# Kernel tuning notes

Measured on AMD Instinct MI355X. Metric: run time of the kernel, lower is better.

## Reference

```python
import jax, jax.numpy as jnp
import numpy as np

N, E, H = 50000, 500000, 4
DIN, DH, DO, TD = 135, 128, 64, 9

def _ln(x, g, b):
    mu = jnp.mean(x, axis=-1, keepdims=True)
    v = jnp.var(x, axis=-1, keepdims=True)
    return (x - mu) / jnp.sqrt(v + 1e-5) * g + b

def _gat(x, src, dst, W, a_src, a_dst, b, n, heads, c):
    h = (x @ W).reshape(n, heads, c)                      # [N,H,C]
    es = jnp.sum(h * a_src, -1)                           # [N,H]
    ed = jnp.sum(h * a_dst, -1)
    e = jax.nn.leaky_relu(es[src] + ed[dst], 0.2)         # [E,H]
    m = jax.ops.segment_max(e, dst, num_segments=n)       # segment softmax over dst
    ex = jnp.exp(e - m[dst])
    den = jax.ops.segment_sum(ex, dst, num_segments=n)
    alpha = ex / (den[dst] + 1e-16)
    out = jax.ops.segment_sum(h[src] * alpha[..., None], dst, num_segments=n)
    return jnp.mean(out, axis=1) + b                      # concat=False -> head mean

def setup_inputs() -> dict:
    key = jax.random.key(0)
    ks = jax.random.split(key, 32)
    rn = lambda i, shape: jax.random.normal(ks[i], shape, jnp.float32) * 0.05
    inp = {}
    inp['x'] = jax.random.normal(ks[0], (N, DIN), jnp.float32)
    inp['edge_index'] = jax.random.randint(ks[1], (2, E), 0, N, jnp.int32)
    inp['edge_attr'] = jnp.ones((E, 1), jnp.float32)
    inp['W_in'] = rn(2, (DIN, DH)); inp['b_in'] = jnp.zeros((DH,), jnp.float32)
    inp['g1W'] = rn(3, (DH, H * DH)); inp['g1as'] = rn(4, (H, DH)); inp['g1ad'] = rn(5, (H, DH)); inp['g1b'] = jnp.zeros((DH,), jnp.float32)
    inp['g2W'] = rn(6, (DH, H * DH)); inp['g2as'] = rn(7, (H, DH)); inp['g2ad'] = rn(8, (H, DH)); inp['g2b'] = jnp.zeros((DH,), jnp.float32)
    inp['g3W'] = rn(9, (DH, H * DO)); inp['g3as'] = rn(10, (H, DO)); inp['g3ad'] = rn(11, (H, DO)); inp['g3b'] = jnp.zeros((DO,), jnp.float32)
    inp['r1W'] = rn(12, (DH, DH)); inp['r1b'] = jnp.zeros((DH,), jnp.float32)
    inp['r2W'] = rn(13, (DH, DH)); inp['r2b'] = jnp.zeros((DH,), jnp.float32)
    inp['r3W'] = rn(14, (DH, DO)); inp['r3b'] = jnp.zeros((DO,), jnp.float32)
    inp['n1g'] = jnp.ones((DH,), jnp.float32); inp['n1b'] = jnp.zeros((DH,), jnp.float32)
    inp['n2g'] = jnp.ones((DH,), jnp.float32); inp['n2b'] = jnp.zeros((DH,), jnp.float32)
    inp['n3g'] = jnp.ones((DO,), jnp.float32); inp['n3b'] = jnp.zeros((DO,), jnp.float32)
    inp['tw'] = jnp.float32(0.3)
    inp['c1W'] = rn(15, (DO, DO)); inp['c1b'] = jnp.zeros((DO,), jnp.float32)
    inp['clg'] = jnp.ones((DO,), jnp.float32); inp['clb'] = jnp.zeros((DO,), jnp.float32)
    inp['c2W'] = rn(16, (DO, 2)); inp['c2b'] = jnp.zeros((2,), jnp.float32)
    return inp

def reference(x, edge_index, edge_attr, W_in, b_in, g1W, g1as, g1ad, g1b,
              g2W, g2as, g2ad, g2b, g3W, g3as, g3ad, g3b,
              r1W, r1b, r2W, r2b, r3W, r3b,
              n1g, n1b, n2g, n2b, n3g, n3b, tw,
              c1W, c1b, clg, clb, c2W, c2b):
    n = x.shape[0]
    src0, dst0 = edge_index[0], edge_index[1]
    loop = jnp.arange(n, dtype=edge_index.dtype)          # GATConv add_self_loops=True
    src = jnp.concatenate([src0, loop])
    dst = jnp.concatenate([dst0, loop])
    # vectorized temporal cosine similarity over original edges
    t = x[:, -TD:]
    ti, tj = t[src0], t[dst0]
    nrm = jnp.maximum(jnp.linalg.norm(ti, axis=-1), 1e-8) * jnp.maximum(jnp.linalg.norm(tj, axis=-1), 1e-8)
    sim = jnp.sum(ti * tj, -1) / nrm
    scale = 1.0 + 0.1 * jnp.mean(1.0 + tw * sim)
    h = x @ W_in + b_in
    id1 = h
    h = _gat(h, src, dst, g1W, g1as, g1ad, g1b, n, H, DH) * scale
    h = _ln(jax.nn.relu(h) + id1 @ r1W + r1b, n1g, n1b)
    id2 = h
    h = _gat(h, src, dst, g2W, g2as, g2ad, g2b, n, H, DH) * scale
    h = _ln(jax.nn.relu(h) + id2 @ r2W + r2b, n2g, n2b)
    id3 = h
    h = _gat(h, src, dst, g3W, g3as, g3ad, g3b, n, H, DO)
    h = _ln(jax.nn.relu(h) + id3 @ r3W + r3b, n3g, n3b)
    ego = h[0:1]
    z = jax.nn.relu(ego @ c1W + c1b)
    z = _ln(z, clg, clb)
    return z @ c2W + c2b
```

## Files before the change

kernel.cpp:

```cpp
#include <hip/hip_runtime.h>

#define AGENT __HIP_MEMORY_SCOPE_AGENT

constexpr int TD = 9, DIN = 135;
constexpr int CAP3 = 256, CAP2 = 1024, CAP1 = 4096, BK = 128;
constexpr int NB = 512;
constexpr int LSTRIDE = 32;
constexpr int NGRP = 16, GSZ = 32;
constexpr int NSET = 8;
constexpr int NLINE = 64;

struct P {
  const float* x; const int* src; const int* dst; int N; int E;
  const float *W_in,*b_in,*g1W,*g1as,*g1ad,*g1b,*g2W,*g2as,*g2ad,*g2b,*g3W,*g3as,*g3ad,*g3b;
  const float *r1W,*r1b,*r2W,*r2b,*r3W,*r3b,*n1g,*n1b,*n2g,*n2b,*n3g,*n3b;
  const float *tw,*c1W,*c1b,*clg,*clb,*c2W,*c2b;
  float* tp;
  int *m3,*m2,*m1,*list3,*list2,*list1,*cnts;
  int *barc,*barr,*barg;
  int *bcnt1,*bcnt2,*bcnt3,*bk1,*bk2,*bk3;
  float *h0,*hh1,*es1,*ed1,*h1,*hh2,*es2,*ed2,*h2,*hh3,*es3,*ed3,*h3;
  float* dout;
};

__device__ __forceinline__ float lrelu(float v) { return v >= 0.f ? v : 0.2f * v; }

__device__ __forceinline__ void stg(float* pp, float v) { __hip_atomic_store(pp, v, __ATOMIC_RELAXED, AGENT); }
__device__ __forceinline__ void stg(int* pp, int v)   { __hip_atomic_store(pp, v, __ATOMIC_RELAXED, AGENT); }

__device__ __forceinline__ void claim_node(int v, int* __restrict__ m, int* __restrict__ list,
                                           int* __restrict__ cnt, int cap) {
  if (atomicCAS(&m[v], -1, -2) == -1) {
    int pos = atomicAdd(cnt, 1);
    if (pos < cap) { stg(&list[pos], v); stg(&m[v], pos); } else { stg(&m[v], -3); }
  }
}

__device__ __forceinline__ void grid_barrier(const P& p, int& lgen, int* amroot_s) {
  __syncthreads();
  int g = lgen + 1;
  if (threadIdx.x == 0) {
    *amroot_s = 0;
    int grp = blockIdx.x & (NGRP - 1);
    int* gc = &p.barc[(((g & (NSET - 1)) * NGRP) + grp) * LSTRIDE];
    if (__hip_atomic_fetch_add(gc, 1, __ATOMIC_RELAXED, AGENT) == GSZ - 1) {
      int* rc = &p.barr[(g & (NSET - 1)) * LSTRIDE];
      if (__hip_atomic_fetch_add(rc, 1, __ATOMIC_RELAXED, AGENT) == NGRP - 1) *amroot_s = 1;
    }
  }
  __syncthreads();
  if (*amroot_s) {
    if (threadIdx.x < NLINE)
      __hip_atomic_store(&p.barg[threadIdx.x * LSTRIDE], g, __ATOMIC_RELAXED, AGENT);
  } else if (threadIdx.x == 0) {
    int* line = &p.barg[(blockIdx.x & (NLINE - 1)) * LSTRIDE];
    while (__hip_atomic_load(line, __ATOMIC_RELAXED, AGENT) < g)
      __builtin_amdgcn_s_sleep(8);
  }
  __syncthreads();
  lgen = g;
}

__global__ void k_init(P p) {
  int gt = blockIdx.x * blockDim.x + threadIdx.x;
  int GT = gridDim.x * blockDim.x;
  int n3 = 3 * p.N;
  int4* mv = (int4*)p.m3;
  int4 neg = make_int4(-1, -1, -1, -1);
  int nv = n3 >> 2;
  for (int i = gt; i < nv; i += GT) mv[i] = neg;
  for (int i = (nv << 2) + gt; i < n3; i += GT) p.m3[i] = -1;
  if (gt < 64) p.cnts[gt] = 0;
  for (int i = gt; i < NSET * NGRP * LSTRIDE; i += GT) p.barc[i] = 0;
  for (int i = gt; i < NSET * LSTRIDE; i += GT) p.barr[i] = 0;
  for (int i = gt; i < NLINE * LSTRIDE; i += GT) p.barg[i] = 0;
  for (int i = gt; i < CAP2; i += GT) p.bcnt1[i] = 0;
  for (int i = gt; i < CAP3; i += GT) p.bcnt2[i] = 0;
  if (gt == 0) p.bcnt3[0] = 0;
  int total = p.N * TD;
  for (int i = gt; i < total; i += GT) {
    int v = i / TD, k = i - v * TD;
    p.tp[i] = p.x[(size_t)v * DIN + (DIN - TD) + k];
  }
}

template <int C, int ONEXT>
__device__ void gat_phase(int nq, const int* lst, const int* mPrev,
                          const int* bket, const int* bcnt,
                          const float* hh, const float* es, const float* ed, const float* hres,
                          const float* gb, const float* rW, const float* rb,
                          const float* ng, const float* nbv, float scale,
                          float* hout, const float* Wn, const float* avn, const float* bvn,
                          float* hhn, float* esn, float* edn,
                          float* elog, int* eposs, float* sh, float* hres_s, float* shln,
                          float* psn, float* pdn, float* sc2, float* ev_s) {
  const int T = 256, Wd = 4 * C, R = Wd / T;
  int tid = threadIdx.x;
  for (int q = blockIdx.x; q < nq; q += gridDim.x) {
    int v = lst[q];
    int sp = mPrev[v];
    int nb = min(bcnt[q], BK);
    for (int j = tid; j < nb; j += T) {
      int pu = mPrev[bket[(size_t)q * BK + j]];
      eposs[j] = pu;
      const float* ep = &es[(size_t)pu * 4];
      elog[0 * BK + j] = ep[0]; elog[1 * BK + j] = ep[1];
      elog[2 * BK + j] = ep[2]; elog[3 * BK + j] = ep[3];
    }
    if (tid < 4) { ev_s[tid] = es[(size_t)sp * 4 + tid]; ev_s[4 + tid] = ed[(size_t)sp * 4 + tid]; }
    for (int k = tid; k < 128; k += T) hres_s[k] = hres[(size_t)sp * 128 + k];
    __syncthreads();
#pragma unroll
    for (int r = 0; r < R; r++) {
      int w = r * T + tid, a = w / C;
      float edv = ev_s[4 + a];
      float eself = lrelu(ev_s[a] + edv);
      float mx = eself;
      for (int j = 0; j < nb; j++) mx = fmaxf(mx, lrelu(elog[a * BK + j] + edv));
      float den = __expf(eself - mx);
      for (int j = 0; j < nb; j++) den += __expf(lrelu(elog[a * BK + j] + edv) - mx);
      float rden = 1.f / (den + 1e-16f);
      float s = __expf(eself - mx) * rden * hh[(size_t)sp * Wd + w];
      for (int j = 0; j < nb; j++)
        s += __expf(lrelu(elog[a * BK + j] + edv) - mx) * rden * hh[(size_t)eposs[j] * Wd + w];
      sh[w] = s;
    }
    __syncthreads();
    float val = 0.f;
    if (tid < C) {
      float g = 0.25f * (sh[tid] + sh[C + tid] + sh[2 * C + tid] + sh[3 * C + tid]) + gb[tid];
      g *= scale;
      g = fmaxf(g, 0.f);
      float rr = rb[tid];
      for (int k = 0; k < 128; k++) rr += hres_s[k] * rW[(size_t)k * C + tid];
      val = g + rr;
      shln[tid] = val;
    }
    __syncthreads();
    if (tid == 0) {
      float s1 = 0.f, s2 = 0.f;
      for (int k = 0; k < C; k++) { float u = shln[k]; s1 += u; s2 += u * u; }
      float mu = s1 / (float)C;
      sc2[0] = mu;
      sc2[1] = rsqrtf(fmaxf(s2 / (float)C - mu * mu, 0.f) + 1e-5f);
    }
    __syncthreads();
    if (tid < C) {
      float o = (val - sc2[0]) * sc2[1] * ng[tid] + nbv[tid];
      stg(&hout[(size_t)q * C + tid], o);
      shln[tid] = o;
    }
    __syncthreads();
    if (ONEXT > 0) {
      for (int j = tid; j < ONEXT; j += T) {
        float a2 = 0.f;
        for (int k = 0; k < C; k++) a2 += shln[k] * Wn[(size_t)k * ONEXT + j];
        stg(&hhn[(size_t)q * ONEXT + j], a2);
        psn[j] = a2 * avn[j]; pdn[j] = a2 * bvn[j];
      }
      __syncthreads();
      if (tid < 8) {
        const int CN = ONEXT / 4; int a = tid & 3;
        const float* pr = (tid < 4) ? psn : pdn;
        float s = 0.f;
        for (int c = 0; c < CN; c++) s += pr[a * CN + c];
        stg(&(tid < 4 ? esn : edn)[(size_t)q * 4 + a], s);
      }
    }
    __syncthreads();
  }
}

__global__ __launch_bounds__(256, 2) void k_mega(P p) {
  __shared__ float elog[4 * BK];
  __shared__ int   eposs[BK];
  __shared__ float sh[512];
  __shared__ float hres_s[128];
  __shared__ float shln[128];
  __shared__ float psn[512], pdn[512];
  __shared__ float xs[DIN + 1];
  __shared__ float sc2[2];
  __shared__ float ev_s[8];
  __shared__ float wred[4];
  __shared__ float zcl[64];
  __shared__ int   amroot_s;

  int tid = threadIdx.x, bid = blockIdx.x;
  int gt = bid * 256 + tid, GT = gridDim.x * 256;
  int lgen = 0;
  float* simsum = (float*)&p.cnts[8];

  {
    if (gt == 0) claim_node(0, p.m3, p.list3, &p.cnts[0], CAP3);
    float local = 0.f;
    for (int e = gt; e < p.E; e += GT) {
      int s = p.src[e], d = p.dst[e];
      if (d == 0) claim_node(s, p.m3, p.list3, &p.cnts[0], CAP3);
      const float* ti = p.tp + (size_t)s * TD;
      const float* tj = p.tp + (size_t)d * TD;
      float dot = 0.f, na = 0.f, nb2 = 0.f;
#pragma unroll
      for (int k = 0; k < TD; k++) { float a = ti[k], b = tj[k]; dot += a * b; na += a * a; nb2 += b * b; }
      local += dot / (fmaxf(sqrtf(na), 1e-8f) * fmaxf(sqrtf(nb2), 1e-8f));
    }
    for (int off = 32; off > 0; off >>= 1) local += __shfl_down(local, off, 64);
    if ((tid & 63) == 0) wred[tid >> 6] = local;
    __syncthreads();
    if (tid == 0) atomicAdd(simsum, wred[0] + wred[1] + wred[2] + wred[3]);
  }
  grid_barrier(p, lgen, &amroot_s);

  {
    int c3 = min(__hip_atomic_load(&p.cnts[0], __ATOMIC_RELAXED, AGENT), CAP3);
    for (int i = gt; i < c3; i += GT) claim_node(p.list3[i], p.m2, p.list2, &p.cnts[1], CAP2);
    for (int e = gt; e < p.E; e += GT)
      if (p.m3[p.dst[e]] >= 0) claim_node(p.src[e], p.m2, p.list2, &p.cnts[1], CAP2);
  }
  grid_barrier(p, lgen, &amroot_s);

  {
    int c2 = min(__hip_atomic_load(&p.cnts[1], __ATOMIC_RELAXED, AGENT), CAP2);
    for (int i = gt; i < c2; i += GT) claim_node(p.list2[i], p.m1, p.list1, &p.cnts[2], CAP1);
    for (int e = gt; e < p.E; e += GT) {
      int s = p.src[e], d = p.dst[e];
      int p2 = p.m2[d];
      if (p2 >= 0) {
        claim_node(s, p.m1, p.list1, &p.cnts[2], CAP1);
        int sl = atomicAdd(&p.bcnt1[p2], 1); if (sl < BK) stg(&p.bk1[(size_t)p2 * BK + sl], s);
      }
      int p3 = p.m3[d];
      if (p3 >= 0) { int sl = atomicAdd(&p.bcnt2[p3], 1); if (sl < BK) stg(&p.bk2[(size_t)p3 * BK + sl], s); }
      if (d == 0)  { int sl = atomicAdd(&p.bcnt3[0], 1);  if (sl < BK) stg(&p.bk3[sl], s); }
    }
  }
  grid_barrier(p, lgen, &amroot_s);

  {
    int c1 = min(__hip_atomic_load(&p.cnts[2], __ATOMIC_RELAXED, AGENT), CAP1);
    for (int pp = bid; pp < c1; pp += gridDim.x) {
      int v = p.list1[pp];
      for (int k = tid; k < DIN; k += 256) xs[k] = p.x[(size_t)v * DIN + k];
      __syncthreads();
      if (tid < 128) {
        float acc = p.b_in[tid];
        for (int k = 0; k < DIN; k++) acc += xs[k] * p.W_in[(size_t)k * 128 + tid];
        stg(&p.h0[(size_t)pp * 128 + tid], acc);
        hres_s[tid] = acc;
      }
      __syncthreads();
#pragma unroll
      for (int jj = 0; jj < 2; jj++) {
        int j = jj * 256 + tid;
        float acc = 0.f;
        for (int k = 0; k < 128; k++) acc += hres_s[k] * p.g1W[(size_t)k * 512 + j];
        stg(&p.hh1[(size_t)pp * 512 + j], acc);
        psn[j] = acc * p.g1as[j]; pdn[j] = acc * p.g1ad[j];
      }
      __syncthreads();
      if (tid < 8) {
        int a = tid & 3;
        const float* pr = (tid < 4) ? psn : pdn;
        float s = 0.f;
        for (int c = 0; c < 128; c++) s += pr[a * 128 + c];
        stg(&(tid < 4 ? p.es1 : p.ed1)[(size_t)pp * 4 + a], s);
      }
      __syncthreads();
    }
  }
  grid_barrier(p, lgen, &amroot_s);

  int sbits = __hip_atomic_load(&p.cnts[8], __ATOMIC_RELAXED, AGENT);
  float scale = 1.1f + 0.1f * p.tw[0] * __int_as_float(sbits) / (float)p.E;

  {
    int c2 = min(__hip_atomic_load(&p.cnts[1], __ATOMIC_RELAXED, AGENT), CAP2);
    gat_phase<128, 512>(c2, p.list2, p.m1, p.bk1, p.bcnt1,
                        p.hh1, p.es1, p.ed1, p.h0,
                        p.g1b, p.r1W, p.r1b, p.n1g, p.n1b, scale,
                        p.h1, p.g2W, p.g2as, p.g2ad, p.hh2, p.es2, p.ed2,
                        elog, eposs, sh, hres_s, shln, psn, pdn, sc2, ev_s);
  }
  grid_barrier(p, lgen, &amroot_s);

  {
    int c3 = min(__hip_atomic_load(&p.cnts[0], __ATOMIC_RELAXED, AGENT), CAP3);
    gat_phase<128, 256>(c3, p.list3, p.m2, p.bk2, p.bcnt2,
                        p.hh2, p.es2, p.ed2, p.h1,
                        p.g2b, p.r2W, p.r2b, p.n2g, p.n2b, scale,
                        p.h2, p.g3W, p.g3as, p.g3ad, p.hh3, p.es3, p.ed3,
                        elog, eposs, sh, hres_s, shln, psn, pdn, sc2, ev_s);
  }
  grid_barrier(p, lgen, &amroot_s);

  {
    gat_phase<64, 0>(1, &p.cnts[56] , p.m3, p.bk3, p.bcnt3,
                     p.hh3, p.es3, p.ed3, p.h2,
                     p.g3b, p.r3W, p.r3b, p.n3g, p.n3b, 1.f,
                     p.h3, nullptr, nullptr, nullptr, nullptr, nullptr, nullptr,
                     elog, eposs, sh, hres_s, shln, psn, pdn, sc2, ev_s);
    if (bid == 0) {
      if (tid < 64) {
        float az = p.c1b[tid];
        for (int k = 0; k < 64; k++) az += shln[k] * p.c1W[k * 64 + tid];
        zcl[tid] = fmaxf(az, 0.f);
      }
      __syncthreads();
      if (tid == 0) {
        float s1 = 0.f, s2 = 0.f;
        for (int k = 0; k < 64; k++) { float u = zcl[k]; s1 += u; s2 += u * u; }
        float mu = s1 / 64.f;
        float rstd = rsqrtf(fmaxf(s2 / 64.f - mu * mu, 0.f) + 1e-5f);
        float o0 = p.c2b[0], o1 = p.c2b[1];
        for (int k = 0; k < 64; k++) {
          float zn = (zcl[k] - mu) * rstd * p.clg[k] + p.clb[k];
          o0 += zn * p.c2W[k * 2 + 0];
          o1 += zn * p.c2W[k * 2 + 1];
        }
        p.dout[0] = o0; p.dout[1] = o1;
      }
    }
  }
}

extern "C" void kernel_launch(void* const* d_in, const int* in_sizes, int n_in,
                              void* d_out, int out_size, void* d_ws, size_t ws_size,
                              hipStream_t stream) {
  P p;
  p.x = (const float*)d_in[0];
  const int* ei = (const int*)d_in[1];
  p.N = in_sizes[0] / DIN;
  p.E = in_sizes[1] / 2;
  p.src = ei; p.dst = ei + p.E;
  p.W_in = (const float*)d_in[3]; p.b_in = (const float*)d_in[4];
  p.g1W = (const float*)d_in[5]; p.g1as = (const float*)d_in[6]; p.g1ad = (const float*)d_in[7]; p.g1b = (const float*)d_in[8];
  p.g2W = (const float*)d_in[9]; p.g2as = (const float*)d_in[10]; p.g2ad = (const float*)d_in[11]; p.g2b = (const float*)d_in[12];
  p.g3W = (const float*)d_in[13]; p.g3as = (const float*)d_in[14]; p.g3ad = (const float*)d_in[15]; p.g3b = (const float*)d_in[16];
  p.r1W = (const float*)d_in[17]; p.r1b = (const float*)d_in[18];
  p.r2W = (const float*)d_in[19]; p.r2b = (const float*)d_in[20];
  p.r3W = (const float*)d_in[21]; p.r3b = (const float*)d_in[22];
  p.n1g = (const float*)d_in[23]; p.n1b = (const float*)d_in[24];
  p.n2g = (const float*)d_in[25]; p.n2b = (const float*)d_in[26];
  p.n3g = (const float*)d_in[27]; p.n3b = (const float*)d_in[28];
  p.tw  = (const float*)d_in[29];
  p.c1W = (const float*)d_in[30]; p.c1b = (const float*)d_in[31];
  p.clg = (const float*)d_in[32]; p.clb = (const float*)d_in[33];
  p.c2W = (const float*)d_in[34]; p.c2b = (const float*)d_in[35];
  p.dout = (float*)d_out;

  char* B = (char*)d_ws;
  size_t off = 0;
  auto take = [&](size_t nbytes) -> char* {
    char* r = B + off;
    off += (nbytes + 255) & ~(size_t)255;
    return r;
  };
  p.cnts  = (int*)take(256);
  p.barc  = (int*)take((size_t)NSET * NGRP * LSTRIDE * 4);
  p.barr  = (int*)take((size_t)NSET * LSTRIDE * 4);
  p.barg  = (int*)take((size_t)NLINE * LSTRIDE * 4);
  p.m3    = (int*)take((size_t)3 * p.N * 4);
  p.m2 = p.m3 + p.N; p.m1 = p.m2 + p.N;
  p.tp    = (float*)take((size_t)p.N * TD * 4);
  p.list3 = (int*)take(CAP3 * 4);
  p.list2 = (int*)take(CAP2 * 4);
  p.list1 = (int*)take(CAP1 * 4);
  p.bcnt1 = (int*)take(CAP2 * 4);
  p.bcnt2 = (int*)take(CAP3 * 4);
  p.bcnt3 = (int*)take(64);
  p.bk1   = (int*)take((size_t)CAP2 * BK * 4);
  p.bk2   = (int*)take((size_t)CAP3 * BK * 4);
  p.bk3   = (int*)take(BK * 4);
  p.h0    = (float*)take((size_t)CAP1 * 128 * 4);
  p.hh1   = (float*)take((size_t)CAP1 * 512 * 4);
  p.es1   = (float*)take((size_t)CAP1 * 16);
  p.ed1   = (float*)take((size_t)CAP1 * 16);
  p.h1    = (float*)take((size_t)CAP2 * 128 * 4);
  p.hh2   = (float*)take((size_t)CAP2 * 512 * 4);
  p.es2   = (float*)take((size_t)CAP2 * 16);
  p.ed2   = (float*)take((size_t)CAP2 * 16);
  p.h2    = (float*)take((size_t)CAP3 * 128 * 4);
  p.hh3   = (float*)take((size_t)CAP3 * 256 * 4);
  p.es3   = (float*)take((size_t)CAP3 * 16);
  p.ed3   = (float*)take((size_t)CAP3 * 16);
  p.h3    = (float*)take(64 * 4);

  k_init<<<1024, 256, 0, stream>>>(p);
  k_mega<<<NB, 256, 0, stream>>>(p);
}
```

Before: 127.5 us.

## Vectorize edge scans, use shared bitsets for frontier tests, batch layer-1 projections

Edge scans now read src/dst as int4 and unroll four edges per thread. Frontier membership is tested against a per-block shared-memory bitset instead of the global m3/m2 maps. The layer-1 input and GAT projections process four nodes per block iteration, so each weight load is reused four times. Grid size, group count and launch bounds are doubled for more occupancy. The 6.4KB bitset plus larger shared buffers may conflict with four blocks per CU, and the bitset assumes N ≤ 51200.

```diff
diff --git a/kernel.cpp b/kernel.cpp
--- a/kernel.cpp
+++ b/kernel.cpp
@@ -4,11 +4,12 @@
 
 constexpr int TD = 9, DIN = 135;
 constexpr int CAP3 = 256, CAP2 = 1024, CAP1 = 4096, BK = 128;
-constexpr int NB = 512;
+constexpr int NB = 1024;
 constexpr int LSTRIDE = 32;
-constexpr int NGRP = 16, GSZ = 32;
+constexpr int NGRP = 32, GSZ = 32;
 constexpr int NSET = 8;
 constexpr int NLINE = 64;
+constexpr int NW32 = 1600;
 
 struct P {
   const float* x; const int* src; const int* dst; int N; int E;
@@ -171,19 +172,21 @@
   }
 }
 
-__global__ __launch_bounds__(256, 2) void k_mega(P p) {
+__global__ __launch_bounds__(256, 4) void k_mega(P p) {
   __shared__ float elog[4 * BK];
   __shared__ int   eposs[BK];
   __shared__ float sh[512];
   __shared__ float hres_s[128];
   __shared__ float shln[128];
   __shared__ float psn[512], pdn[512];
-  __shared__ float xs[DIN + 1];
   __shared__ float sc2[2];
   __shared__ float ev_s[8];
   __shared__ float wred[4];
   __shared__ float zcl[64];
   __shared__ int   amroot_s;
+  __shared__ unsigned int bs[NW32];
+  __shared__ float xs4[4][DIN + 1];
+  __shared__ float hs4[4][128];
 
   int tid = threadIdx.x, bid = blockIdx.x;
   int gt = bid * 256 + tid, GT = gridDim.x * 256;
@@ -193,13 +196,32 @@
   {
     if (gt == 0) claim_node(0, p.m3, p.list3, &p.cnts[0], CAP3);
     float local = 0.f;
-    for (int e = gt; e < p.E; e += GT) {
+    int nq4 = p.E >> 2;
+    const int4* s4p = (const int4*)p.src;
+    const int4* d4p = (const int4*)p.dst;
+    for (int q = gt; q < nq4; q += GT) {
+      int4 s4 = s4p[q];
+      int4 d4 = d4p[q];
+      int ss[4] = {s4.x, s4.y, s4.z, s4.w};
+      int dd[4] = {d4.x, d4.y, d4.z, d4.w};
+#pragma unroll
+      for (int u = 0; u < 4; u++) {
+        int s = ss[u], d = dd[u];
+        if (d == 0) claim_node(s, p.m3, p.list3, &p.cnts[0], CAP3);
+        const float* ti = p.tp + (size_t)s * TD;
+        const float* tj = p.tp + (size_t)d * TD;
+        float dot = 0.f, na = 0.f, nb2 = 0.f;
+#pragma unroll
+        for (int k = 0; k < TD; k++) { float a = ti[k], b = tj[k]; dot += a * b; na += a * a; nb2 += b * b; }
+        local += dot / (fmaxf(sqrtf(na), 1e-8f) * fmaxf(sqrtf(nb2), 1e-8f));
+      }
+    }
+    for (int e = (nq4 << 2) + gt; e < p.E; e += GT) {
       int s = p.src[e], d = p.dst[e];
       if (d == 0) claim_node(s, p.m3, p.list3, &p.cnts[0], CAP3);
       const float* ti = p.tp + (size_t)s * TD;
       const float* tj = p.tp + (size_t)d * TD;
       float dot = 0.f, na = 0.f, nb2 = 0.f;
-#pragma unroll
       for (int k = 0; k < TD; k++) { float a = ti[k], b = tj[k]; dot += a * b; na += a * a; nb2 += b * b; }
       local += dot / (fmaxf(sqrtf(na), 1e-8f) * fmaxf(sqrtf(nb2), 1e-8f));
     }
@@ -211,60 +233,141 @@
   grid_barrier(p, lgen, &amroot_s);
 
   {
+    for (int i = tid; i < NW32; i += 256) bs[i] = 0u;
+    __syncthreads();
     int c3 = min(__hip_atomic_load(&p.cnts[0], __ATOMIC_RELAXED, AGENT), CAP3);
+    for (int i = tid; i < c3; i += 256) {
+      int v = p.list3[i];
+      atomicOr(&bs[v >> 5], 1u << (v & 31));
+    }
+    __syncthreads();
     for (int i = gt; i < c3; i += GT) claim_node(p.list3[i], p.m2, p.list2, &p.cnts[1], CAP2);
-    for (int e = gt; e < p.E; e += GT)
-      if (p.m3[p.dst[e]] >= 0) claim_node(p.src[e], p.m2, p.list2, &p.cnts[1], CAP2);
-  }
-  grid_barrier(p, lgen, &amroot_s);
-
-  {
+    int nq4 = p.E >> 2;
+    const int4* s4p = (const int4*)p.src;
+    const int4* d4p = (const int4*)p.dst;
+    for (int q = gt; q < nq4; q += GT) {
+      int4 s4 = s4p[q];
+      int4 d4 = d4p[q];
+      int ss[4] = {s4.x, s4.y, s4.z, s4.w};
+      int dd[4] = {d4.x, d4.y, d4.z, d4.w};
+#pragma unroll
+      for (int u = 0; u < 4; u++) {
+        int d = dd[u];
+        if (bs[d >> 5] & (1u << (d & 31)))
+          claim_node(ss[u], p.m2, p.list2, &p.cnts[1], CAP2);
+      }
+    }
+    for (int e = (nq4 << 2) + gt; e < p.E; e += GT) {
+      int d = p.dst[e];
+      if (bs[d >> 5] & (1u << (d & 31)))
+        claim_node(p.src[e], p.m2, p.list2, &p.cnts[1], CAP2);
+    }
+  }
+  grid_barrier(p, lgen, &amroot_s);
+
+  {
+    for (int i = tid; i < NW32; i += 256) bs[i] = 0u;
+    __syncthreads();
     int c2 = min(__hip_atomic_load(&p.cnts[1], __ATOMIC_RELAXED, AGENT), CAP2);
+    for (int i = tid; i < c2; i += 256) {
+      int v = p.list2[i];
+      atomicOr(&bs[v >> 5], 1u << (v & 31));
+    }
+    __syncthreads();
     for (int i = gt; i < c2; i += GT) claim_node(p.list2[i], p.m1, p.list1, &p.cnts[2], CAP1);
-    for (int e = gt; e < p.E; e += GT) {
+    int nq4 = p.E >> 2;
+    const int4* s4p = (const int4*)p.src;
+    const int4* d4p = (const int4*)p.dst;
+    for (int q = gt; q < nq4; q += GT) {
+      int4 s4 = s4p[q];
+      int4 d4 = d4p[q];
+      int ss[4] = {s4.x, s4.y, s4.z, s4.w};
+      int dd[4] = {d4.x, d4.y, d4.z, d4.w};
+#pragma unroll
+      for (int u = 0; u < 4; u++) {
+        int s = ss[u], d = dd[u];
+        if (bs[d >> 5] & (1u << (d & 31))) {
+          claim_node(s, p.m1, p.list1, &p.cnts[2], CAP1);
+          int p2 = p.m2[d];
+          int sl = atomicAdd(&p.bcnt1[p2], 1); if (sl < BK) stg(&p.bk1[(size_t)p2 * BK + sl], s);
+          int p3 = p.m3[d];
+          if (p3 >= 0) { int sl2 = atomicAdd(&p.bcnt2[p3], 1); if (sl2 < BK) stg(&p.bk2[(size_t)p3 * BK + sl2], s); }
+          if (d == 0)  { int sl3 = atomicAdd(&p.bcnt3[0], 1);  if (sl3 < BK) stg(&p.bk3[sl3], s); }
+        }
+      }
+    }
+    for (int e = (nq4 << 2) + gt; e < p.E; e += GT) {
       int s = p.src[e], d = p.dst[e];
-      int p2 = p.m2[d];
-      if (p2 >= 0) {
+      if (bs[d >> 5] & (1u << (d & 31))) {
         claim_node(s, p.m1, p.list1, &p.cnts[2], CAP1);
+        int p2 = p.m2[d];
         int sl = atomicAdd(&p.bcnt1[p2], 1); if (sl < BK) stg(&p.bk1[(size_t)p2 * BK + sl], s);
-      }
-      int p3 = p.m3[d];
-      if (p3 >= 0) { int sl = atomicAdd(&p.bcnt2[p3], 1); if (sl < BK) stg(&p.bk2[(size_t)p3 * BK + sl], s); }
-      if (d == 0)  { int sl = atomicAdd(&p.bcnt3[0], 1);  if (sl < BK) stg(&p.bk3[sl], s); }
+        int p3 = p.m3[d];
+        if (p3 >= 0) { int sl2 = atomicAdd(&p.bcnt2[p3], 1); if (sl2 < BK) stg(&p.bk2[(size_t)p3 * BK + sl2], s); }
+        if (d == 0)  { int sl3 = atomicAdd(&p.bcnt3[0], 1);  if (sl3 < BK) stg(&p.bk3[sl3], s); }
+      }
     }
   }
   grid_barrier(p, lgen, &amroot_s);
 
   {
     int c1 = min(__hip_atomic_load(&p.cnts[2], __ATOMIC_RELAXED, AGENT), CAP1);
-    for (int pp = bid; pp < c1; pp += gridDim.x) {
-      int v = p.list1[pp];
-      for (int k = tid; k < DIN; k += 256) xs[k] = p.x[(size_t)v * DIN + k];
+    int ng4 = (c1 + 3) >> 2;
+    for (int g4 = bid; g4 < ng4; g4 += gridDim.x) {
+      int base = g4 * 4;
+      int cnt4 = min(4, c1 - base);
+      for (int u = 0; u < cnt4; u++) {
+        int v = p.list1[base + u];
+        for (int k = tid; k < DIN; k += 256) xs4[u][k] = p.x[(size_t)v * DIN + k];
+      }
       __syncthreads();
       if (tid < 128) {
-        float acc = p.b_in[tid];
-        for (int k = 0; k < DIN; k++) acc += xs[k] * p.W_in[(size_t)k * 128 + tid];
-        stg(&p.h0[(size_t)pp * 128 + tid], acc);
-        hres_s[tid] = acc;
+        float a0 = p.b_in[tid], a1 = a0, a2 = a0, a3 = a0;
+        for (int k = 0; k < DIN; k++) {
+          float w = p.W_in[(size_t)k * 128 + tid];
+          a0 += xs4[0][k] * w; a1 += xs4[1][k] * w; a2 += xs4[2][k] * w; a3 += xs4[3][k] * w;
+        }
+        hs4[0][tid] = a0; hs4[1][tid] = a1; hs4[2][tid] = a2; hs4[3][tid] = a3;
+        if (0 < cnt4) stg(&p.h0[(size_t)(base + 0) * 128 + tid], a0);
+        if (1 < cnt4) stg(&p.h0[(size_t)(base + 1) * 128 + tid], a1);
+        if (2 < cnt4) stg(&p.h0[(size_t)(base + 2) * 128 + tid], a2);
+        if (3 < cnt4) stg(&p.h0[(size_t)(base + 3) * 128 + tid], a3);
       }
       __syncthreads();
+      float b4[2][4];
 #pragma unroll
       for (int jj = 0; jj < 2; jj++) {
         int j = jj * 256 + tid;
-        float acc = 0.f;
-        for (int k = 0; k < 128; k++) acc += hres_s[k] * p.g1W[(size_t)k * 512 + j];
-        stg(&p.hh1[(size_t)pp * 512 + j], acc);
-        psn[j] = acc * p.g1as[j]; pdn[j] = acc * p.g1ad[j];
-      }
-      __syncthreads();
-      if (tid < 8) {
-        int a = tid & 3;
-        const float* pr = (tid < 4) ? psn : pdn;
-        float s = 0.f;
-        for (int c = 0; c < 128; c++) s += pr[a * 128 + c];
-        stg(&(tid < 4 ? p.es1 : p.ed1)[(size_t)pp * 4 + a], s);
-      }
-      __syncthreads();
+        float b0 = 0.f, b1 = 0.f, b2 = 0.f, b3 = 0.f;
+        for (int k = 0; k < 128; k++) {
+          float w = p.g1W[(size_t)k * 512 + j];
+          b0 += hs4[0][k] * w; b1 += hs4[1][k] * w; b2 += hs4[2][k] * w; b3 += hs4[3][k] * w;
+        }
+        b4[jj][0] = b0; b4[jj][1] = b1; b4[jj][2] = b2; b4[jj][3] = b3;
+        if (0 < cnt4) stg(&p.hh1[(size_t)(base + 0) * 512 + j], b0);
+        if (1 < cnt4) stg(&p.hh1[(size_t)(base + 1) * 512 + j], b1);
+        if (2 < cnt4) stg(&p.hh1[(size_t)(base + 2) * 512 + j], b2);
+        if (3 < cnt4) stg(&p.hh1[(size_t)(base + 3) * 512 + j], b3);
+      }
+#pragma unroll
+      for (int u = 0; u < 4; u++) {
+        if (u >= cnt4) break;
+#pragma unroll
+        for (int jj = 0; jj < 2; jj++) {
+          int j = jj * 256 + tid;
+          psn[j] = b4[jj][u] * p.g1as[j];
+          pdn[j] = b4[jj][u] * p.g1ad[j];
+        }
+        __syncthreads();
+        if (tid < 8) {
+          int a = tid & 3;
+          const float* pr = (tid < 4) ? psn : pdn;
+          float s = 0.f;
+          for (int c = 0; c < 128; c++) s += pr[a * 128 + c];
+          stg(&(tid < 4 ? p.es1 : p.ed1)[(size_t)(base + u) * 4 + a], s);
+        }
+        __syncthreads();
+      }
     }
   }
   grid_barrier(p, lgen, &amroot_s);
```

New measurement: 251.5 us. +97.3%, slower.
